# Kernel optimization log

Hardware: AMD Instinct MI355X
Metric: run time of the kernel (lower is better)

Reference implementation:

```python
import jax, jax.numpy as jnp
import numpy as np

TOP_K = 8  # num_experts_per_tok


def setup_inputs() -> dict:
    key = jax.random.key(0)
    k1, k2 = jax.random.split(key)
    hidden_states = jax.random.normal(k1, (4, 4096, 2048), dtype=jnp.float32)
    weight = jax.random.normal(k2, (128, 2048), dtype=jnp.float32) * 0.02
    return {"hidden_states": hidden_states, "weight": weight}


def reference(hidden_states, weight):
    B, S, H = hidden_states.shape
    x = hidden_states.reshape(-1, H).astype(jnp.float32)        # [T, H], T = B*S
    logits = jnp.einsum("th,eh->te", x, weight.astype(jnp.float32))  # [T, E]
    scores = jax.nn.softmax(logits, axis=-1)                    # float32 softmax
    topk_weight, topk_idx = jax.lax.top_k(scores, TOP_K)        # [T, K]
    # norm_topk_prob=True: renormalize selected probabilities
    topk_weight = topk_weight / jnp.sum(topk_weight, axis=-1, keepdims=True)
    return topk_idx, topk_weight
```

## Files before the change

### kernel.cpp

```cpp
#include <hip/hip_runtime.h>
#include <math.h>

#define T_TOKENS 16384
#define HDIM     2048
#define NEXP     128
#define TOPK     8

#define BK    64
#define NCH   (HDIM / BK)
#define TM    32

#define F16_MIN_NORM    6.1035156e-05f
#define SPLIT_SCALE     4096.0f
#define INV_SPLIT_SCALE 2.44140625e-04f

typedef __attribute__((ext_vector_type(8))) _Float16 f16x8;
typedef __attribute__((ext_vector_type(4))) float    f32x4;

__device__ __forceinline__ void f16split(float f, _Float16& hi, _Float16& lo) {
    _Float16 h = (_Float16)f;
    float back = (float)h;
    if (fabsf(f) < F16_MIN_NORM) { h = (_Float16)0.f; back = 0.f; }
    lo = (_Float16)((f - back) * SPLIT_SCALE);
    hi = h;
}

__global__ __launch_bounds__(256) void pack_w(const float* __restrict__ w,
                                              unsigned short* __restrict__ wp1,
                                              unsigned short* __restrict__ wp2) {
    int p = blockIdx.x * 256 + threadIdx.x;
    int lane = p & 63, nt = (p >> 6) & 7, kk = p >> 9;
    int col = lane & 15, quad = lane >> 4;
    const float* src = w + (size_t)(nt * 16 + col) * HDIM + kk * 32 + quad * 8;
    unsigned short h[8], l[8];
#pragma unroll
    for (int j = 0; j < 8; ++j) {
        _Float16 hh, ll;
        f16split(src[j], hh, ll);
        union { _Float16 x; unsigned short u; } ch, cl;
        ch.x = hh; cl.x = ll;
        h[j] = ch.u; l[j] = cl.u;
    }
    *(uint4*)(wp1 + (size_t)p * 8) = *(const uint4*)h;
    *(uint4*)(wp2 + (size_t)p * 8) = *(const uint4*)l;
}

struct ARegs { f32x4 v[8]; };
struct BRegs { f16x8 v[8]; };

__global__ __launch_bounds__(256, 2) void moe_gate(const float* __restrict__ x,
                                                   const unsigned short* __restrict__ wp1,
                                                   const unsigned short* __restrict__ wp2,
                                                   float* __restrict__ out_idx,
                                                   float* __restrict__ out_w) {
    __shared__ __align__(16) float epil[TM * 132];

    const int tid  = threadIdx.x;
    const int lane = tid & 63;
    const int wv   = tid >> 6;
    const int col  = lane & 15;
    const int quad = lane >> 4;
    const long tok0 = (long)blockIdx.x * TM;

    const float* xg = x + (tok0 + col) * (long)HDIM + quad * 8;

    f32x4 acc[2][2], accc[2][2];
#pragma unroll
    for (int m = 0; m < 2; ++m)
#pragma unroll
        for (int j = 0; j < 2; ++j) { acc[m][j] = (f32x4){0,0,0,0}; accc[m][j] = (f32x4){0,0,0,0}; }

    f16x8 af1[2][2], af2[2][2];

    auto loadA = [&](int ch, ARegs& A) {
#pragma unroll
        for (int m = 0; m < 2; ++m) {
            const float* p = xg + (size_t)m * 16 * HDIM + ch * BK;
            A.v[m * 4 + 0] = *(const f32x4*)(p);
            A.v[m * 4 + 1] = *(const f32x4*)(p + 4);
            A.v[m * 4 + 2] = *(const f32x4*)(p + 32);
            A.v[m * 4 + 3] = *(const f32x4*)(p + 36);
        }
    };
    auto loadB = [&](int ch, BRegs& B) {
        const size_t cho = (size_t)ch * 8192;
#pragma unroll
        for (int kk = 0; kk < 2; ++kk)
#pragma unroll
            for (int j = 0; j < 2; ++j) {
                const size_t o = cho + (size_t)(((kk * 8) + (wv * 2 + j)) * 64 + lane) * 8;
                B.v[(kk * 2 + j) * 2 + 0] = *(const f16x8*)(wp1 + o);
                B.v[(kk * 2 + j) * 2 + 1] = *(const f16x8*)(wp2 + o);
            }
    };
    auto splitA = [&](ARegs& A) {
#pragma unroll
        for (int m = 0; m < 2; ++m)
#pragma unroll
            for (int kk = 0; kk < 2; ++kk) {
                f32x4 v0 = A.v[m * 4 + kk * 2 + 0];
                f32x4 v1 = A.v[m * 4 + kk * 2 + 1];
#pragma unroll
                for (int j = 0; j < 8; ++j) {
                    float f = (j < 4) ? v0[j] : v1[j - 4];
                    _Float16 hh, ll;
                    f16split(f, hh, ll);
                    af1[kk][m][j] = hh;
                    af2[kk][m][j] = ll;
                }
            }
    };
    auto mfmaStep = [&](BRegs& B) {
#pragma unroll
        for (int kk = 0; kk < 2; ++kk)
#pragma unroll
            for (int j = 0; j < 2; ++j) {
                f16x8 bf1 = B.v[(kk * 2 + j) * 2 + 0];
                f16x8 bf2 = B.v[(kk * 2 + j) * 2 + 1];
#pragma unroll
                for (int m = 0; m < 2; ++m) {
                    acc[m][j]  = __builtin_amdgcn_mfma_f32_16x16x32_f16(af1[kk][m], bf1, acc[m][j],  0, 0, 0);
                    accc[m][j] = __builtin_amdgcn_mfma_f32_16x16x32_f16(af1[kk][m], bf2, accc[m][j], 0, 0, 0);
                    accc[m][j] = __builtin_amdgcn_mfma_f32_16x16x32_f16(af2[kk][m], bf1, accc[m][j], 0, 0, 0);
                }
            }
    };

    ARegs A0, A1;
    BRegs B0, B1;

    loadA(0, A0); loadB(0, B0);

    for (int ch = 0; ch < NCH; ch += 2) {
        if (ch + 1 < NCH) { loadA(ch + 1, A1); loadB(ch + 1, B1); }
        splitA(A0);
        mfmaStep(B0);
        if (ch + 2 < NCH) { loadA(ch + 2, A0); loadB(ch + 2, B0); }
        if (ch + 1 < NCH) { splitA(A1); mfmaStep(B1); }
    }

#pragma unroll
    for (int m = 0; m < 2; ++m)
#pragma unroll
        for (int j = 0; j < 2; ++j)
#pragma unroll
            for (int r = 0; r < 4; ++r)
                epil[(m * 16 + quad * 4 + r) * 132 + (wv * 2 + j) * 16 + col] =
                    acc[m][j][r] + accc[m][j][r] * INV_SPLIT_SCALE;
    __syncthreads();

    for (int i = 0; i < 8; ++i) {
        const int t = wv * 8 + i;
        float2 p = *(const float2*)(epil + t * 132 + 2 * lane);
        float v0 = p.x, v1 = p.y;
        const int i0 = 2 * lane, i1 = 2 * lane + 1;

        float topv[TOPK];
        int topi[TOPK];
#pragma unroll
        for (int s = 0; s < TOPK; ++s) {
            float mv = (v0 >= v1) ? v0 : v1;
            int   mi = (v0 >= v1) ? i0 : i1;
#pragma unroll
            for (int off = 32; off >= 1; off >>= 1) {
                float ov = __shfl_xor(mv, off);
                int   oi = __shfl_xor(mi, off);
                if (ov > mv || (ov == mv && oi < mi)) { mv = ov; mi = oi; }
            }
            topv[s] = mv; topi[s] = mi;
            if (i0 == mi) v0 = -INFINITY;
            if (i1 == mi) v1 = -INFINITY;
        }

        const float m = topv[0];
        float sum = 0.f;
#pragma unroll
        for (int s = 0; s < TOPK; ++s) sum += expf(topv[s] - m);
        const float inv = 1.f / sum;

        float myv = topv[0]; int myi = topi[0];
#pragma unroll
        for (int s = 1; s < TOPK; ++s)
            if (lane == s) { myv = topv[s]; myi = topi[s]; }

        if (lane < TOPK) {
            long tok = tok0 + t;
            out_idx[tok * TOPK + lane] = (float)myi;
            out_w[tok * TOPK + lane]   = expf(myv - m) * inv;
        }
    }
}

extern "C" void kernel_launch(void* const* d_in, const int* in_sizes, int n_in,
                              void* d_out, int out_size, void* d_ws, size_t ws_size,
                              hipStream_t stream) {
    const float* x = (const float*)d_in[0];
    const float* w = (const float*)d_in[1];
    float* out = (float*)d_out;

    unsigned short* wp1 = (unsigned short*)d_ws;
    unsigned short* wp2 = wp1 + (size_t)NEXP * HDIM;

    pack_w<<<(64 * 8 * 64) / 256, 256, 0, stream>>>(w, wp1, wp2);
    moe_gate<<<T_TOKENS / TM, 256, 0, stream>>>(x, wp1, wp2, out, out + (size_t)T_TOKENS * TOPK);
}
```

Baseline: 284.6 us.

## Stage split A tile in swizzled LDS shared across waves with double buffering

Before, each of the four waves loaded the full 32x64 fp32 A tile per chunk and split it into f16 hi/lo itself, so the same global loads and split arithmetic were repeated four times. Now every thread loads and splits only 8 floats, writes the hi/lo halves into a swizzled, double-buffered LDS tile, and the waves read their MFMA fragments from LDS. Ping-pong buffers are separated by lgkmcnt waits and barriers. This removes redundant global traffic and ALU work and lowers register pressure, at the cost of LDS round trips and a barrier per chunk.

```diff
diff --git a/kernel.cpp b/kernel.cpp
--- a/kernel.cpp
+++ b/kernel.cpp
@@ -16,6 +16,8 @@
 
 typedef __attribute__((ext_vector_type(8))) _Float16 f16x8;
 typedef __attribute__((ext_vector_type(4))) float    f32x4;
+
+#define LGKM0()   asm volatile("s_waitcnt lgkmcnt(0)" ::: "memory")
 
 __device__ __forceinline__ void f16split(float f, _Float16& hi, _Float16& lo) {
     _Float16 h = (_Float16)f;
@@ -23,6 +25,10 @@
     if (fabsf(f) < F16_MIN_NORM) { h = (_Float16)0.f; back = 0.f; }
     lo = (_Float16)((f - back) * SPLIT_SCALE);
     hi = h;
+}
+
+__device__ __forceinline__ int swz(int b) {
+    return b ^ (((b >> 8) & 3) << 4) ^ (((b >> 11) & 1) << 6);
 }
 
 __global__ __launch_bounds__(256) void pack_w(const float* __restrict__ w,
@@ -45,7 +51,6 @@
     *(uint4*)(wp2 + (size_t)p * 8) = *(const uint4*)l;
 }
 
-struct ARegs { f32x4 v[8]; };
 struct BRegs { f16x8 v[8]; };
 
 __global__ __launch_bounds__(256, 2) void moe_gate(const float* __restrict__ x,
@@ -53,7 +58,8 @@
                                                    const unsigned short* __restrict__ wp2,
                                                    float* __restrict__ out_idx,
                                                    float* __restrict__ out_w) {
-    __shared__ __align__(16) float epil[TM * 132];
+    __shared__ __align__(16) unsigned char smem[17408];
+    float* epil = (float*)smem;
 
     const int tid  = threadIdx.x;
     const int lane = tid & 63;
@@ -62,7 +68,10 @@
     const int quad = lane >> 4;
     const long tok0 = (long)blockIdx.x * TM;
 
-    const float* xg = x + (tok0 + col) * (long)HDIM + quad * 8;
+    const int srow = tid >> 3, skseg = tid & 7;
+    const float* xgs = x + (tok0 + srow) * (long)HDIM + skseg * 8;
+    const int acell = (((skseg >> 2) * 2 + (srow >> 4)) * 64 + (skseg & 3) * 16 + (srow & 15));
+    const int adst  = swz(acell * 16);
 
     f32x4 acc[2][2], accc[2][2];
 #pragma unroll
@@ -70,17 +79,25 @@
 #pragma unroll
         for (int j = 0; j < 2; ++j) { acc[m][j] = (f32x4){0,0,0,0}; accc[m][j] = (f32x4){0,0,0,0}; }
 
-    f16x8 af1[2][2], af2[2][2];
-
-    auto loadA = [&](int ch, ARegs& A) {
-#pragma unroll
-        for (int m = 0; m < 2; ++m) {
-            const float* p = xg + (size_t)m * 16 * HDIM + ch * BK;
-            A.v[m * 4 + 0] = *(const f32x4*)(p);
-            A.v[m * 4 + 1] = *(const f32x4*)(p + 4);
-            A.v[m * 4 + 2] = *(const f32x4*)(p + 32);
-            A.v[m * 4 + 3] = *(const f32x4*)(p + 36);
-        }
+    f32x4 Av0, Av1;
+
+    auto loadA = [&](int ch) {
+        Av0 = *(const f32x4*)(xgs + ch * BK);
+        Av1 = *(const f32x4*)(xgs + ch * BK + 4);
+    };
+    auto splitWriteA = [&](int b) {
+        unsigned short h[8], l[8];
+#pragma unroll
+        for (int j = 0; j < 8; ++j) {
+            _Float16 hh, ll;
+            f16split(j < 4 ? Av0[j] : Av1[j - 4], hh, ll);
+            union { _Float16 x; unsigned short u; } ch_, cl_;
+            ch_.x = hh; cl_.x = ll;
+            h[j] = ch_.u; l[j] = cl_.u;
+        }
+        unsigned char* base = smem + b * 8192;
+        *(uint4*)(base + adst)        = *(const uint4*)h;
+        *(uint4*)(base + 4096 + adst) = *(const uint4*)l;
     };
     auto loadB = [&](int ch, BRegs& B) {
         const size_t cho = (size_t)ch * 8192;
@@ -93,51 +110,62 @@
                 B.v[(kk * 2 + j) * 2 + 1] = *(const f16x8*)(wp2 + o);
             }
     };
-    auto splitA = [&](ARegs& A) {
-#pragma unroll
-        for (int m = 0; m < 2; ++m)
-#pragma unroll
-            for (int kk = 0; kk < 2; ++kk) {
-                f32x4 v0 = A.v[m * 4 + kk * 2 + 0];
-                f32x4 v1 = A.v[m * 4 + kk * 2 + 1];
-#pragma unroll
-                for (int j = 0; j < 8; ++j) {
-                    float f = (j < 4) ? v0[j] : v1[j - 4];
-                    _Float16 hh, ll;
-                    f16split(f, hh, ll);
-                    af1[kk][m][j] = hh;
-                    af2[kk][m][j] = ll;
-                }
-            }
-    };
-    auto mfmaStep = [&](BRegs& B) {
-#pragma unroll
-        for (int kk = 0; kk < 2; ++kk)
+    auto mfmaStep = [&](int b, BRegs& B) {
+        const unsigned char* base = smem + b * 8192;
+#pragma unroll
+        for (int kk = 0; kk < 2; ++kk) {
+            f16x8 af1v[2], af2v[2];
+#pragma unroll
+            for (int m = 0; m < 2; ++m) {
+                const int bo = swz(((kk * 2 + m) * 64 + lane) * 16);
+                af1v[m] = *(const f16x8*)(base + bo);
+                af2v[m] = *(const f16x8*)(base + 4096 + bo);
+            }
 #pragma unroll
             for (int j = 0; j < 2; ++j) {
                 f16x8 bf1 = B.v[(kk * 2 + j) * 2 + 0];
                 f16x8 bf2 = B.v[(kk * 2 + j) * 2 + 1];
 #pragma unroll
                 for (int m = 0; m < 2; ++m) {
-                    acc[m][j]  = __builtin_amdgcn_mfma_f32_16x16x32_f16(af1[kk][m], bf1, acc[m][j],  0, 0, 0);
-                    accc[m][j] = __builtin_amdgcn_mfma_f32_16x16x32_f16(af1[kk][m], bf2, accc[m][j], 0, 0, 0);
-                    accc[m][j] = __builtin_amdgcn_mfma_f32_16x16x32_f16(af2[kk][m], bf1, accc[m][j], 0, 0, 0);
+                    acc[m][j]  = __builtin_amdgcn_mfma_f32_16x16x32_f16(af1v[m], bf1, acc[m][j],  0, 0, 0);
+                    accc[m][j] = __builtin_amdgcn_mfma_f32_16x16x32_f16(af1v[m], bf2, accc[m][j], 0, 0, 0);
+                    accc[m][j] = __builtin_amdgcn_mfma_f32_16x16x32_f16(af2v[m], bf1, accc[m][j], 0, 0, 0);
                 }
             }
-    };
-
-    ARegs A0, A1;
+        }
+    };
+
     BRegs B0, B1;
 
-    loadA(0, A0); loadB(0, B0);
-
-    for (int ch = 0; ch < NCH; ch += 2) {
-        if (ch + 1 < NCH) { loadA(ch + 1, A1); loadB(ch + 1, B1); }
-        splitA(A0);
-        mfmaStep(B0);
-        if (ch + 2 < NCH) { loadA(ch + 2, A0); loadB(ch + 2, B0); }
-        if (ch + 1 < NCH) { splitA(A1); mfmaStep(B1); }
+    loadA(0);
+    loadB(0, B0);
+    loadB(1, B1);
+    splitWriteA(0);
+    loadA(1);
+    LGKM0();
+    __builtin_amdgcn_s_barrier();
+
+    for (int ch = 0; ch < NCH - 2; ch += 2) {
+        splitWriteA(1);
+        loadA(ch + 2);
+        mfmaStep(0, B0);
+        loadB(ch + 2, B0);
+        LGKM0();
+        __builtin_amdgcn_s_barrier();
+
+        splitWriteA(0);
+        loadA(ch + 3);
+        mfmaStep(1, B1);
+        loadB(ch + 3, B1);
+        LGKM0();
+        __builtin_amdgcn_s_barrier();
     }
+    splitWriteA(1);
+    mfmaStep(0, B0);
+    LGKM0();
+    __builtin_amdgcn_s_barrier();
+    mfmaStep(1, B1);
+    __syncthreads();
 
 #pragma unroll
     for (int m = 0; m < 2; ++m)
```

Result: faster. 248.2 us (-12.8%).
